# Optimization experiments

Measured on AMD Instinct MI355X. Metric: run time of the kernel, lower is better.

## Reference

```python
import jax, jax.numpy as jnp
import numpy as np

UNITS = 1024
N_CLASSES = 16
F_IN = 128
LN_EPS = 1e-3  # keras LayerNormalization default epsilon


def _lstm_cell(x, h, c, W, U, b):
    # keras LSTMCell gate order: i, f, g(candidate), o
    z = x @ W + h @ U + b  # [B, 4U]
    i, f, g, o = jnp.split(z, 4, axis=-1)
    i = jax.nn.sigmoid(i)
    f = jax.nn.sigmoid(f)
    g = jnp.tanh(g)
    o = jax.nn.sigmoid(o)
    c_new = f * c + i * g
    h_new = o * jnp.tanh(c_new)
    return h_new, c_new


def _layernorm(x, gamma, beta):
    mu = jnp.mean(x, axis=-1, keepdims=True)
    var = jnp.mean(jnp.square(x - mu), axis=-1, keepdims=True)
    return (x - mu) * jax.lax.rsqrt(var + LN_EPS) * gamma + beta


def setup_inputs() -> dict:
    key = jax.random.key(0)
    ks = jax.random.split(key, 8)
    s = 0.02
    inp = {
        "inputs": jax.random.normal(ks[0], (64, 512, F_IN), dtype=jnp.float32),
        "W0": jax.random.normal(ks[1], (F_IN, 4 * UNITS), dtype=jnp.float32) * s,
        "U0": jax.random.normal(ks[2], (UNITS, 4 * UNITS), dtype=jnp.float32) * s,
        "b0": jnp.zeros((4 * UNITS,), jnp.float32),
        "g0": jnp.ones((UNITS,), jnp.float32),
        "be0": jnp.zeros((UNITS,), jnp.float32),
        "W1": jax.random.normal(ks[3], (UNITS, 4 * UNITS), dtype=jnp.float32) * s,
        "U1": jax.random.normal(ks[4], (UNITS, 4 * UNITS), dtype=jnp.float32) * s,
        "b1": jnp.zeros((4 * UNITS,), jnp.float32),
        "g1": jnp.ones((UNITS,), jnp.float32),
        "be1": jnp.zeros((UNITS,), jnp.float32),
        "Wfc": jax.random.normal(ks[5], (UNITS, N_CLASSES), dtype=jnp.float32) * s,
        "bfc": jnp.zeros((N_CLASSES,), jnp.float32),
    }
    return inp


def reference(inputs, W0, U0, b0, g0, be0, W1, U1, b1, g1, be1, Wfc, bfc):
    B = inputs.shape[0]
    x_t = jnp.transpose(inputs, (1, 0, 2))  # [T, B, F]
    h0 = jnp.zeros((B, UNITS), jnp.float32)
    c0 = jnp.zeros((B, UNITS), jnp.float32)
    h1 = jnp.zeros((B, UNITS), jnp.float32)
    c1 = jnp.zeros((B, UNITS), jnp.float32)

    def step(carry, xt):
        h0, c0, h1, c1 = carry
        # layer 0: raw (h, c) carried across time; normalized output feeds layer 1
        h0n, c0n = _lstm_cell(xt, h0, c0, W0, U0, b0)
        o0 = _layernorm(h0n, g0, be0)
        h1n, c1n = _lstm_cell(o0, h1, c1, W1, U1, b1)
        o1 = _layernorm(h1n, g1, be1)
        # dropout is identity at inference (training=False)
        logits = jax.nn.softmax(o1 @ Wfc + bfc, axis=-1)
        return (h0n, c0n, h1n, c1n), logits

    _, out = jax.lax.scan(step, (h0, c0, h1, c1), x_t)  # [T, B, C]
    return jnp.transpose(out, (1, 0, 2))  # [B, T, C]
```

## Files before the change

### kernel.cpp

```cpp
#include <hip/hip_runtime.h>

typedef unsigned short u16;
typedef unsigned int u32;
typedef unsigned long long u64;
typedef __bf16 bf16x8 __attribute__((ext_vector_type(8)));
typedef float f32x4 __attribute__((ext_vector_type(4)));

#define T_LEN 512
#define BATCH 64
#define FIN 128
#define UNITS 1024

#define O_BAR   0
#define SZ_BAR  8192
#define O_XBF   SZ_BAR
#define SZ_XBF  (T_LEN*BATCH*FIN*2)
#define O_WP0   (O_XBF + SZ_XBF)
#define SZ_WP0  (1152*4096*2)
#define O_WP1   (O_WP0 + SZ_WP0)
#define SZ_WP1  (2048*4096*2)
#define O_WFC   (O_WP1 + SZ_WP1)
#define SZ_WFC  (16*1024*2)
#define O_H0    (O_WFC + SZ_WFC)
#define SZ_H    (BATCH*UNITS*2)
#define O_H1    (O_H0 + SZ_H)
#define WS_NEED (O_H1 + SZ_H)

__device__ __forceinline__ float bf2f(u16 s) {
  u32 u = ((u32)s) << 16;
  return __builtin_bit_cast(float, u);
}
__device__ __forceinline__ u16 f2bf(float f) {
  u32 u = __builtin_bit_cast(u32, f);
  u32 r = (u + 0x7FFFu + ((u >> 16) & 1u)) >> 16;
  return (u16)r;
}
__device__ __forceinline__ float sigm(float x) { return 1.0f / (1.0f + __expf(-x)); }
__device__ __forceinline__ float tanhft(float x) { return 1.0f - 2.0f / (__expf(2.0f * x) + 1.0f); }

__device__ __forceinline__ uint4 ldh16(const u16* q) {
  u64 a = __hip_atomic_load((const u64*)q,     __ATOMIC_RELAXED, __HIP_MEMORY_SCOPE_AGENT);
  u64 b = __hip_atomic_load((const u64*)q + 1, __ATOMIC_RELAXED, __HIP_MEMORY_SCOPE_AGENT);
  uint4 r; r.x = (u32)a; r.y = (u32)(a >> 32); r.z = (u32)b; r.w = (u32)(b >> 32);
  return r;
}
__device__ __forceinline__ void sth(u16* q, u16 v) {
  __hip_atomic_store(q, v, __ATOMIC_RELAXED, __HIP_MEMORY_SCOPE_AGENT);
}

__global__ void k_zero(u32* p, int n) {
  int i = blockIdx.x * 256 + threadIdx.x;
  if (i < n) p[i] = 0u;
}

__global__ void k_pack_x(const float* __restrict__ src, u16* __restrict__ dst) {
  int i = blockIdx.x * 256 + threadIdx.x;
  int f = i & 127, tb = i >> 7;
  int b = tb & 63, t = tb >> 6;
  dst[i] = f2bf(src[(b * T_LEN + t) * FIN + f]);
}

__global__ void k_pack_w0(const float* __restrict__ W0, const float* __restrict__ U0,
                          u16* __restrict__ dst) {
  int i = blockIdx.x * 256 + threadIdx.x;
  int j = i & 7, lane = (i >> 3) & 63, rest = i >> 9;
  int ktg = rest % 36, tmp = rest / 36;
  int nt = tmp & 3, ug = tmp >> 2;
  int k = ktg * 32 + ((lane >> 4) << 3) + j;
  int rr = nt * 16 + (lane & 15);
  int gate = rr & 3, ul = rr >> 2;
  int col = gate * 1024 + ug * 16 + ul;
  float v = (k < FIN) ? W0[k * 4096 + col] : U0[(k - FIN) * 4096 + col];
  dst[i] = f2bf(v);
}

__global__ void k_pack_w1(const float* __restrict__ W1, const float* __restrict__ U1,
                          u16* __restrict__ dst) {
  int i = blockIdx.x * 256 + threadIdx.x;
  int j = i & 7, lane = (i >> 3) & 63, rest = i >> 9;
  int ktg = rest & 63, tmp = rest >> 6;
  int nt = tmp & 3, ug = tmp >> 2;
  int k = ktg * 32 + ((lane >> 4) << 3) + j;
  int rr = nt * 16 + (lane & 15);
  int gate = rr & 3, ul = rr >> 2;
  int col = gate * 1024 + ug * 16 + ul;
  float v = (k < UNITS) ? W1[k * 4096 + col] : U1[(k - UNITS) * 4096 + col];
  dst[i] = f2bf(v);
}

__global__ void k_pack_wfc(const float* __restrict__ Wfc, u16* __restrict__ dst) {
  int i = blockIdx.x * 256 + threadIdx.x;
  int k = i & 1023, c = i >> 10;
  dst[c * 1024 + k] = f2bf(Wfc[k * 16 + c]);
}

struct KP {
  const u16* xbf; const u16* wp0; const u16* wp1; const u16* wfc;
  u16* h0; u16* h1; u32* bar;
  const float* b0; const float* g0; const float* be0;
  const float* b1; const float* g1; const float* be1;
  const float* bfc; float* out;
};

__device__ __forceinline__ void accst(uint4 v, float& s1, float& s2) {
  u32 a[4] = {v.x, v.y, v.z, v.w};
#pragma unroll
  for (int e = 0; e < 4; ++e) {
    float f0 = bf2f((u16)(a[e] & 0xffffu));
    float f1 = bf2f((u16)(a[e] >> 16));
    s1 += f0 + f1;
    s2 += f0 * f0 + f1 * f1;
  }
}

__device__ __forceinline__ uint4 normpack(uint4 v, float mu, float rs,
                                          const float* gg, const float* bb) {
  u32 a[4] = {v.x, v.y, v.z, v.w};
  u32 o[4];
#pragma unroll
  for (int e = 0; e < 4; ++e) {
    float f0 = (bf2f((u16)(a[e] & 0xffffu)) - mu) * rs * gg[2 * e] + bb[2 * e];
    float f1 = (bf2f((u16)(a[e] >> 16)) - mu) * rs * gg[2 * e + 1] + bb[2 * e + 1];
    o[e] = (u32)f2bf(f0) | ((u32)f2bf(f1) << 16);
  }
  uint4 r; r.x = o[0]; r.y = o[1]; r.z = o[2]; r.w = o[3];
  return r;
}

__device__ __forceinline__ void barrier_bg(u32* gen, u32* flags, int ug, int lane,
                                           int wv, u32 ep) {
  __syncthreads();
  if (wv == 0) {
    if (lane == 0)
      __hip_atomic_store(flags + ug * 4, ep, __ATOMIC_RELAXED, __HIP_MEMORY_SCOPE_AGENT);
    if (ug == 0) {
      for (;;) {
        u32 v = __hip_atomic_load(flags + lane * 4, __ATOMIC_RELAXED, __HIP_MEMORY_SCOPE_AGENT);
        if (__ballot(v >= ep) == ~0ull) break;
        __builtin_amdgcn_s_sleep(1);
      }
      if (lane == 0)
        __hip_atomic_store(gen, ep, __ATOMIC_RELAXED, __HIP_MEMORY_SCOPE_AGENT);
    } else if (lane == 0) {
      while (__hip_atomic_load(gen, __ATOMIC_RELAXED, __HIP_MEMORY_SCOPE_AGENT) < ep)
        __builtin_amdgcn_s_sleep(1);
    }
  }
  __syncthreads();
  asm volatile("" ::: "memory");
}

__global__ void __launch_bounds__(512, 2) k_persist(KP p) {
  const int tid = threadIdx.x;
  const int ug = blockIdx.x & 63, bg = blockIdx.x >> 6;
  const int lane = tid & 63, wv = tid >> 6;
  const int nt = wv & 3, kh = wv >> 2;

  __shared__ __align__(16) u16 bufA[16][1032];
  __shared__ __align__(16) u16 bufB[16][1032];
  __shared__ __align__(16) u16 buf0[16][1032];
  __shared__ float zb[2][16][68];
  __shared__ float g0s[1024], be0s[1024];
  __shared__ float b0s[64], b1s[64];
  __shared__ float mu_s[16], sg_s[16];
  __shared__ float lbuf[16];

  for (int i = tid; i < 1024; i += 512) { g0s[i] = p.g0[i]; be0s[i] = p.be0[i]; }
  if (tid < 64) {
    int gate = tid & 3, ul = tid >> 2;
    b0s[tid] = p.b0[gate * 1024 + ug * 16 + ul];
    b1s[tid] = p.b1[gate * 1024 + ug * 16 + ul];
  }
  {
    u32* za = (u32*)&bufA[0][0];
    u32* zc = (u32*)&bufB[0][0];
    for (int i = tid; i < 16 * 1032 / 2; i += 512) { za[i] = 0u; zc[i] = 0u; }
  }
  const float g1a = p.g1[tid * 2], g1b = p.g1[tid * 2 + 1];
  const float be1a = p.be1[tid * 2], be1b = p.be1[tid * 2 + 1];

  bf16x8 w0r[18], w1r[32];
  {
    const u16* q0 = p.wp0 + (size_t)(((ug * 4 + nt) * 36 + kh * 18) * 64 + lane) * 8;
#pragma unroll
    for (int s = 0; s < 18; ++s)
      w0r[s] = __builtin_bit_cast(bf16x8, *(const uint4*)(q0 + (size_t)s * 512));
    const u16* q1 = p.wp1 + (size_t)(((ug * 4 + nt) * 64 + kh * 32) * 64 + lane) * 8;
#pragma unroll
    for (int s = 0; s < 32; ++s)
      w1r[s] = __builtin_bit_cast(bf16x8, *(const uint4*)(q1 + (size_t)s * 512));
  }

  u32* gen   = p.bar + bg * 64;
  u32* flags = p.bar + 256 + bg * 256;

  float c0 = 0.f, c1 = 0.f;
  const int gr = tid >> 4, gu = tid & 15;
  const int srow = tid >> 5, ssub = tid & 31;
  const int am = lane & 15, aq = (lane >> 4) << 3;

  __syncthreads();

  for (int t = 0; t < T_LEN; ++t) {
    const u32 epA = 2 * t + 1, epB = 2 * t + 2;

    f32x4 acc0 = {0.f, 0.f, 0.f, 0.f};
    if (kh == 0) {
      const u16* xr = p.xbf + (size_t)(t * 64 + bg * 16 + am) * FIN + aq;
#pragma unroll
      for (int s = 0; s < 4; ++s) {
        bf16x8 a = __builtin_bit_cast(bf16x8, *(const uint4*)(xr + s * 32));
        acc0 = __builtin_amdgcn_mfma_f32_16x16x32_bf16(a, w0r[s], acc0, 0, 0, 0);
      }
#pragma unroll
      for (int s = 4; s < 18; ++s) {
        bf16x8 a = __builtin_bit_cast(bf16x8, *(const uint4*)&bufA[am][s * 32 + aq - 128]);
        acc0 = __builtin_amdgcn_mfma_f32_16x16x32_bf16(a, w0r[s], acc0, 0, 0, 0);
      }
    } else {
#pragma unroll
      for (int s = 0; s < 18; ++s) {
        bf16x8 a = __builtin_bit_cast(bf16x8, *(const uint4*)&bufA[am][448 + s * 32 + aq]);
        acc0 = __builtin_amdgcn_mfma_f32_16x16x32_bf16(a, w0r[s], acc0, 0, 0, 0);
      }
    }
#pragma unroll
    for (int i = 0; i < 4; ++i)
      zb[kh][(lane >> 4) * 4 + i][nt * 16 + (lane & 15)] = acc0[i];
    __syncthreads();

    if (tid < 256) {
      const float* zr0 = &zb[0][gr][gu * 4];
      const float* zr1 = &zb[1][gr][gu * 4];
      float zi = zr0[0] + zr1[0] + b0s[gu * 4 + 0];
      float zf = zr0[1] + zr1[1] + b0s[gu * 4 + 1];
      float zg = zr0[2] + zr1[2] + b0s[gu * 4 + 2];
      float zo = zr0[3] + zr1[3] + b0s[gu * 4 + 3];
      float gi = sigm(zi), gf = sigm(zf), gg = tanhft(zg), go = sigm(zo);
      c0 = gf * c0 + gi * gg;
      float h = go * tanhft(c0);
      sth(p.h0 + (size_t)(bg * 16 + gr) * UNITS + ug * 16 + gu, f2bf(h));
    }
    barrier_bg(gen, flags, ug, lane, wv, epA);

    {
      const u16* h0r = p.h0 + (size_t)(bg * 16 + srow) * UNITS + ssub * 8;
      uint4 a0 = ldh16(h0r);
      uint4 a1 = ldh16(h0r + 256);
      uint4 a2 = ldh16(h0r + 512);
      uint4 a3 = ldh16(h0r + 768);

      float s1 = 0.f, s2 = 0.f;
      accst(a0, s1, s2); accst(a1, s1, s2); accst(a2, s1, s2); accst(a3, s1, s2);
#pragma unroll
      for (int m = 1; m <= 16; m <<= 1) { s1 += __shfl_xor(s1, m); s2 += __shfl_xor(s2, m); }
      if (ssub == 0) {
        float mu = s1 * (1.0f / 1024.0f);
        float va = s2 * (1.0f / 1024.0f) - mu * mu;
        mu_s[srow] = mu;
        sg_s[srow] = rsqrtf(va + 1e-3f);
      }
      *(uint4*)&bufA[srow][ssub * 8]       = a0;
      *(uint4*)&bufA[srow][256 + ssub * 8] = a1;
      *(uint4*)&bufA[srow][512 + ssub * 8] = a2;
      *(uint4*)&bufA[srow][768 + ssub * 8] = a3;
      __syncthreads();
      float mu = mu_s[srow], rs = sg_s[srow];
      *(uint4*)&buf0[srow][ssub * 8]       = normpack(a0, mu, rs, &g0s[ssub * 8], &be0s[ssub * 8]);
      *(uint4*)&buf0[srow][256 + ssub * 8] = normpack(a1, mu, rs, &g0s[256 + ssub * 8], &be0s[256 + ssub * 8]);
      *(uint4*)&buf0[srow][512 + ssub * 8] = normpack(a2, mu, rs, &g0s[512 + ssub * 8], &be0s[512 + ssub * 8]);
      *(uint4*)&buf0[srow][768 + ssub * 8] = normpack(a3, mu, rs, &g0s[768 + ssub * 8], &be0s[768 + ssub * 8]);
    }
    __syncthreads();

    f32x4 acc1 = {0.f, 0.f, 0.f, 0.f};
    if (kh == 0) {
#pragma unroll
      for (int s = 0; s < 32; ++s) {
        bf16x8 a = __builtin_bit_cast(bf16x8, *(const uint4*)&buf0[am][s * 32 + aq]);
        acc1 = __builtin_amdgcn_mfma_f32_16x16x32_bf16(a, w1r[s], acc1, 0, 0, 0);
      }
    } else {
#pragma unroll
      for (int s = 0; s < 32; ++s) {
        bf16x8 a = __builtin_bit_cast(bf16x8, *(const uint4*)&bufB[am][s * 32 + aq]);
        acc1 = __builtin_amdgcn_mfma_f32_16x16x32_bf16(a, w1r[s], acc1, 0, 0, 0);
      }
    }
#pragma unroll
    for (int i = 0; i < 4; ++i)
      zb[kh][(lane >> 4) * 4 + i][nt * 16 + (lane & 15)] = acc1[i];
    __syncthreads();

    if (tid < 256) {
      const float* zr0 = &zb[0][gr][gu * 4];
      const float* zr1 = &zb[1][gr][gu * 4];
      float zi = zr0[0] + zr1[0] + b1s[gu * 4 + 0];
      float zf = zr0[1] + zr1[1] + b1s[gu * 4 + 1];
      float zg = zr0[2] + zr1[2] + b1s[gu * 4 + 2];
      float zo = zr0[3] + zr1[3] + b1s[gu * 4 + 3];
      float gi = sigm(zi), gf = sigm(zf), gg = tanhft(zg), go = sigm(zo);
      c1 = gf * c1 + gi * gg;
      float h = go * tanhft(c1);
      sth(p.h1 + (size_t)(bg * 16 + gr) * UNITS + ug * 16 + gu, f2bf(h));
    }
    barrier_bg(gen, flags, ug, lane, wv, epB);

    {
      const u16* h1r = p.h1 + (size_t)(bg * 16 + srow) * UNITS + ssub * 8;
      uint4 a0 = ldh16(h1r);
      uint4 a1 = ldh16(h1r + 256);
      uint4 a2 = ldh16(h1r + 512);
      uint4 a3 = ldh16(h1r + 768);
      float s1 = 0.f, s2 = 0.f;
      accst(a0, s1, s2); accst(a1, s1, s2); accst(a2, s1, s2); accst(a3, s1, s2);
#pragma unroll
      for (int m = 1; m <= 16; m <<= 1) { s1 += __shfl_xor(s1, m); s2 += __shfl_xor(s2, m); }
      if (ssub == 0) {
        float mu = s1 * (1.0f / 1024.0f);
        float va = s2 * (1.0f / 1024.0f) - mu * mu;
        mu_s[srow] = mu;
        sg_s[srow] = rsqrtf(va + 1e-3f);
      }
      *(uint4*)&bufB[srow][ssub * 8]       = a0;
      *(uint4*)&bufB[srow][256 + ssub * 8] = a1;
      *(uint4*)&bufB[srow][512 + ssub * 8] = a2;
      *(uint4*)&bufB[srow][768 + ssub * 8] = a3;
    }
    __syncthreads();

    if (ug < 16) {
      const int row = bg * 16 + ug;
      u32 hv = *(const u32*)&bufB[ug][tid * 2];
      float f0 = bf2f((u16)(hv & 0xffffu)), f1 = bf2f((u16)(hv >> 16));
      {
        float mu = mu_s[ug], rs = sg_s[ug];
        float* o1f = (float*)&buf0[0][0];
        o1f[tid * 2]     = (f0 - mu) * rs * g1a + be1a;
        o1f[tid * 2 + 1] = (f1 - mu) * rs * g1b + be1b;
      }
      __syncthreads();
      if (tid < 256) {
        const int cls = tid & 15, ks = tid >> 4;
        const float* o1f = (const float*)&buf0[0][0];
        const u16* wrow = p.wfc + cls * 1024 + ks * 64;
        float pa = 0.f;
#pragma unroll
        for (int q8 = 0; q8 < 8; ++q8) {
          uint4 wv4 = *(const uint4*)(wrow + q8 * 8);
          u32 aa[4] = {wv4.x, wv4.y, wv4.z, wv4.w};
#pragma unroll
          for (int e = 0; e < 4; ++e) {
            int k = ks * 64 + q8 * 8 + e * 2;
            pa += o1f[k]     * bf2f((u16)(aa[e] & 0xffffu));
            pa += o1f[k + 1] * bf2f((u16)(aa[e] >> 16));
          }
        }
        zb[0][ks][cls] = pa;
      }
      __syncthreads();
      if (tid < 16) {
        float lg = p.bfc[tid];
#pragma unroll
        for (int ks = 0; ks < 16; ++ks) lg += zb[0][ks][tid];
        lbuf[tid] = lg;
      }
      __syncthreads();
      if (tid < 16) {
        float mx = lbuf[0];
#pragma unroll
        for (int j2 = 1; j2 < 16; ++j2) mx = fmaxf(mx, lbuf[j2]);
        float ssum = 0.f;
#pragma unroll
        for (int j2 = 0; j2 < 16; ++j2) ssum += __expf(lbuf[j2] - mx);
        p.out[((size_t)row * T_LEN + t) * 16 + tid] = __expf(lbuf[tid] - mx) / ssum;
      }
      __syncthreads();
    }
  }
}

extern "C" void kernel_launch(void* const* d_in, const int* in_sizes, int n_in,
                              void* d_out, int out_size, void* d_ws, size_t ws_size,
                              hipStream_t stream) {
  (void)in_sizes; (void)n_in; (void)out_size;
  if (ws_size < (size_t)WS_NEED) return;

  const float* inp = (const float*)d_in[0];
  const float* W0  = (const float*)d_in[1];
  const float* U0  = (const float*)d_in[2];
  const float* b0  = (const float*)d_in[3];
  const float* g0  = (const float*)d_in[4];
  const float* be0 = (const float*)d_in[5];
  const float* W1  = (const float*)d_in[6];
  const float* U1  = (const float*)d_in[7];
  const float* b1  = (const float*)d_in[8];
  const float* g1  = (const float*)d_in[9];
  const float* be1 = (const float*)d_in[10];
  const float* Wfc = (const float*)d_in[11];
  const float* bfc = (const float*)d_in[12];

  char* ws = (char*)d_ws;
  u32* bar  = (u32*)(ws + O_BAR);
  u16* xbf  = (u16*)(ws + O_XBF);
  u16* wp0  = (u16*)(ws + O_WP0);
  u16* wp1  = (u16*)(ws + O_WP1);
  u16* wfcT = (u16*)(ws + O_WFC);
  u16* h0   = (u16*)(ws + O_H0);
  u16* h1   = (u16*)(ws + O_H1);

  k_zero<<<8, 256, 0, stream>>>(bar, 2048);
  k_pack_x<<<16384, 256, 0, stream>>>(inp, xbf);
  k_pack_w0<<<18432, 256, 0, stream>>>(W0, U0, wp0);
  k_pack_w1<<<32768, 256, 0, stream>>>(W1, U1, wp1);
  k_pack_wfc<<<64, 256, 0, stream>>>(Wfc, wfcT);

  KP p;
  p.xbf = xbf; p.wp0 = wp0; p.wp1 = wp1; p.wfc = wfcT;
  p.h0 = h0; p.h1 = h1; p.bar = bar;
  p.b0 = b0; p.g0 = g0; p.be0 = be0;
  p.b1 = b1; p.g1 = g1; p.be1 = be1;
  p.bfc = bfc; p.out = (float*)d_out;

  void* args[] = { &p };
  hipLaunchCooperativeKernel((const void*)k_persist, dim3(256), dim3(512), args, 0, stream);
}
```

Measured before the change: 7.683 ms.

## Merge per-step grid barriers via double-buffered hidden states and decentralized barrier

Double-buffers the h0/h1 global hidden-state buffers by timestep parity, so the layer-1 state from the previous step can be read after the same barrier that publishes the current layer-0 state. This halves the group-wide barriers per timestep from two to one. The barrier also becomes decentralized: every block polls all flags itself instead of waiting for a leader block to set a generation word. The FC/softmax output is deferred one step, with an epilogue barrier for the last step. The cost is extra polling traffic on the flags from every block and a more subtle ordering argument for buffer reuse across steps.

```diff
diff --git a/kernel.cpp b/kernel.cpp
--- a/kernel.cpp
+++ b/kernel.cpp
@@ -10,6 +10,7 @@
 #define BATCH 64
 #define FIN 128
 #define UNITS 1024
+#define H_STRIDE 65536
 
 #define O_BAR   0
 #define SZ_BAR  8192
@@ -22,7 +23,7 @@
 #define O_WFC   (O_WP1 + SZ_WP1)
 #define SZ_WFC  (16*1024*2)
 #define O_H0    (O_WFC + SZ_WFC)
-#define SZ_H    (BATCH*UNITS*2)
+#define SZ_H    (2*H_STRIDE*2)
 #define O_H1    (O_H0 + SZ_H)
 #define WS_NEED (O_H1 + SZ_H)
 
@@ -127,27 +128,73 @@
   return r;
 }
 
-__device__ __forceinline__ void barrier_bg(u32* gen, u32* flags, int ug, int lane,
-                                           int wv, u32 ep) {
+__device__ __forceinline__ void barrier_bg(u32* flags, int ug, int lane, int wv, u32 ep) {
   __syncthreads();
   if (wv == 0) {
     if (lane == 0)
       __hip_atomic_store(flags + ug * 4, ep, __ATOMIC_RELAXED, __HIP_MEMORY_SCOPE_AGENT);
-    if (ug == 0) {
-      for (;;) {
-        u32 v = __hip_atomic_load(flags + lane * 4, __ATOMIC_RELAXED, __HIP_MEMORY_SCOPE_AGENT);
-        if (__ballot(v >= ep) == ~0ull) break;
-        __builtin_amdgcn_s_sleep(1);
-      }
-      if (lane == 0)
-        __hip_atomic_store(gen, ep, __ATOMIC_RELAXED, __HIP_MEMORY_SCOPE_AGENT);
-    } else if (lane == 0) {
-      while (__hip_atomic_load(gen, __ATOMIC_RELAXED, __HIP_MEMORY_SCOPE_AGENT) < ep)
-        __builtin_amdgcn_s_sleep(1);
+    for (;;) {
+      u32 v = __hip_atomic_load(flags + lane * 4, __ATOMIC_RELAXED, __HIP_MEMORY_SCOPE_AGENT);
+      if (__ballot(v >= ep) == ~0ull) break;
+      __builtin_amdgcn_s_sleep(1);
     }
   }
   __syncthreads();
   asm volatile("" ::: "memory");
+}
+
+__device__ __forceinline__ void fc_out(int tid, int ug, int bg, int t,
+    u16 (*bufB)[1032], u16 (*buf0)[1032], float (*zb0)[68],
+    const float* mu_s, const float* sg_s, float* lbuf,
+    float g1a, float g1b, float be1a, float be1b,
+    const u16* __restrict__ wfc, const float* __restrict__ bfc,
+    float* __restrict__ out) {
+  const int row = bg * 16 + ug;
+  u32 hv = *(const u32*)&bufB[ug][tid * 2];
+  float f0 = bf2f((u16)(hv & 0xffffu)), f1 = bf2f((u16)(hv >> 16));
+  {
+    float mu = mu_s[ug], rs = sg_s[ug];
+    float* o1f = (float*)&buf0[0][0];
+    o1f[tid * 2]     = (f0 - mu) * rs * g1a + be1a;
+    o1f[tid * 2 + 1] = (f1 - mu) * rs * g1b + be1b;
+  }
+  __syncthreads();
+  if (tid < 256) {
+    const int cls = tid & 15, ks = tid >> 4;
+    const float* o1f = (const float*)&buf0[0][0];
+    const u16* wrow = wfc + cls * 1024 + ks * 64;
+    float pa = 0.f;
+#pragma unroll
+    for (int q8 = 0; q8 < 8; ++q8) {
+      uint4 wv4 = *(const uint4*)(wrow + q8 * 8);
+      u32 aa[4] = {wv4.x, wv4.y, wv4.z, wv4.w};
+#pragma unroll
+      for (int e = 0; e < 4; ++e) {
+        int k = ks * 64 + q8 * 8 + e * 2;
+        pa += o1f[k]     * bf2f((u16)(aa[e] & 0xffffu));
+        pa += o1f[k + 1] * bf2f((u16)(aa[e] >> 16));
+      }
+    }
+    zb0[ks][cls] = pa;
+  }
+  __syncthreads();
+  if (tid < 16) {
+    float lg = bfc[tid];
+#pragma unroll
+    for (int ks = 0; ks < 16; ++ks) lg += zb0[ks][tid];
+    lbuf[tid] = lg;
+  }
+  __syncthreads();
+  if (tid < 16) {
+    float mx = lbuf[0];
+#pragma unroll
+    for (int j2 = 1; j2 < 16; ++j2) mx = fmaxf(mx, lbuf[j2]);
+    float ssum = 0.f;
+#pragma unroll
+    for (int j2 = 0; j2 < 16; ++j2) ssum += __expf(lbuf[j2] - mx);
+    out[((size_t)row * T_LEN + t) * 16 + tid] = __expf(lbuf[tid] - mx) / ssum;
+  }
+  __syncthreads();
 }
 
 __global__ void __launch_bounds__(512, 2) k_persist(KP p) {
@@ -173,8 +220,7 @@
   }
   {
     u32* za = (u32*)&bufA[0][0];
-    u32* zc = (u32*)&bufB[0][0];
-    for (int i = tid; i < 16 * 1032 / 2; i += 512) { za[i] = 0u; zc[i] = 0u; }
+    for (int i = tid; i < 16 * 1032 / 2; i += 512) za[i] = 0u;
   }
   const float g1a = p.g1[tid * 2], g1b = p.g1[tid * 2 + 1];
   const float be1a = p.be1[tid * 2], be1b = p.be1[tid * 2 + 1];
@@ -191,8 +237,7 @@
       w1r[s] = __builtin_bit_cast(bf16x8, *(const uint4*)(q1 + (size_t)s * 512));
   }
 
-  u32* gen   = p.bar + bg * 64;
-  u32* flags = p.bar + 256 + bg * 256;
+  u32* flags = p.bar + bg * 256;
 
   float c0 = 0.f, c1 = 0.f;
   const int gr = tid >> 4, gu = tid & 15;
@@ -202,7 +247,7 @@
   __syncthreads();
 
   for (int t = 0; t < T_LEN; ++t) {
-    const u32 epA = 2 * t + 1, epB = 2 * t + 2;
+    const int cur = t & 1, rd = cur ^ 1;
 
     f32x4 acc0 = {0.f, 0.f, 0.f, 0.f};
     if (kh == 0) {
@@ -239,37 +284,53 @@
       float gi = sigm(zi), gf = sigm(zf), gg = tanhft(zg), go = sigm(zo);
       c0 = gf * c0 + gi * gg;
       float h = go * tanhft(c0);
-      sth(p.h0 + (size_t)(bg * 16 + gr) * UNITS + ug * 16 + gu, f2bf(h));
-    }
-    barrier_bg(gen, flags, ug, lane, wv, epA);
+      sth(p.h0 + (size_t)cur * H_STRIDE + (size_t)(bg * 16 + gr) * UNITS + ug * 16 + gu,
+          f2bf(h));
+    }
+    barrier_bg(flags, ug, lane, wv, (u32)(t + 1));
 
     {
-      const u16* h0r = p.h0 + (size_t)(bg * 16 + srow) * UNITS + ssub * 8;
+      const u16* h0r = p.h0 + (size_t)cur * H_STRIDE + (size_t)(bg * 16 + srow) * UNITS + ssub * 8;
+      const u16* h1r = p.h1 + (size_t)rd  * H_STRIDE + (size_t)(bg * 16 + srow) * UNITS + ssub * 8;
       uint4 a0 = ldh16(h0r);
       uint4 a1 = ldh16(h0r + 256);
       uint4 a2 = ldh16(h0r + 512);
       uint4 a3 = ldh16(h0r + 768);
+      uint4 b0 = ldh16(h1r);
+      uint4 b1 = ldh16(h1r + 256);
+      uint4 b2 = ldh16(h1r + 512);
+      uint4 b3 = ldh16(h1r + 768);
 
       float s1 = 0.f, s2 = 0.f;
       accst(a0, s1, s2); accst(a1, s1, s2); accst(a2, s1, s2); accst(a3, s1, s2);
 #pragma unroll
       for (int m = 1; m <= 16; m <<= 1) { s1 += __shfl_xor(s1, m); s2 += __shfl_xor(s2, m); }
-      if (ssub == 0) {
-        float mu = s1 * (1.0f / 1024.0f);
-        float va = s2 * (1.0f / 1024.0f) - mu * mu;
-        mu_s[srow] = mu;
-        sg_s[srow] = rsqrtf(va + 1e-3f);
-      }
+      float mu0 = s1 * (1.0f / 1024.0f);
+      float rs0 = rsqrtf(s2 * (1.0f / 1024.0f) - mu0 * mu0 + 1e-3f);
+
       *(uint4*)&bufA[srow][ssub * 8]       = a0;
       *(uint4*)&bufA[srow][256 + ssub * 8] = a1;
       *(uint4*)&bufA[srow][512 + ssub * 8] = a2;
       *(uint4*)&bufA[srow][768 + ssub * 8] = a3;
-      __syncthreads();
-      float mu = mu_s[srow], rs = sg_s[srow];
-      *(uint4*)&buf0[srow][ssub * 8]       = normpack(a0, mu, rs, &g0s[ssub * 8], &be0s[ssub * 8]);
-      *(uint4*)&buf0[srow][256 + ssub * 8] = normpack(a1, mu, rs, &g0s[256 + ssub * 8], &be0s[256 + ssub * 8]);
-      *(uint4*)&buf0[srow][512 + ssub * 8] = normpack(a2, mu, rs, &g0s[512 + ssub * 8], &be0s[512 + ssub * 8]);
-      *(uint4*)&buf0[srow][768 + ssub * 8] = normpack(a3, mu, rs, &g0s[768 + ssub * 8], &be0s[768 + ssub * 8]);
+
+      float u1 = 0.f, u2 = 0.f;
+      accst(b0, u1, u2); accst(b1, u1, u2); accst(b2, u1, u2); accst(b3, u1, u2);
+#pragma unroll
+      for (int m = 1; m <= 16; m <<= 1) { u1 += __shfl_xor(u1, m); u2 += __shfl_xor(u2, m); }
+      if (ssub == 0) {
+        float mu = u1 * (1.0f / 1024.0f);
+        mu_s[srow] = mu;
+        sg_s[srow] = rsqrtf(u2 * (1.0f / 1024.0f) - mu * mu + 1e-3f);
+      }
+      *(uint4*)&bufB[srow][ssub * 8]       = b0;
+      *(uint4*)&bufB[srow][256 + ssub * 8] = b1;
+      *(uint4*)&bufB[srow][512 + ssub * 8] = b2;
+      *(uint4*)&bufB[srow][768 + ssub * 8] = b3;
+
+      *(uint4*)&buf0[srow][ssub * 8]       = normpack(a0, mu0, rs0, &g0s[ssub * 8], &be0s[ssub * 8]);
+      *(uint4*)&buf0[srow][256 + ssub * 8] = normpack(a1, mu0, rs0, &g0s[256 + ssub * 8], &be0s[256 + ssub * 8]);
+      *(uint4*)&buf0[srow][512 + ssub * 8] = normpack(a2, mu0, rs0, &g0s[512 + ssub * 8], &be0s[512 + ssub * 8]);
+      *(uint4*)&buf0[srow][768 + ssub * 8] = normpack(a3, mu0, rs0, &g0s[768 + ssub * 8], &be0s[768 + ssub * 8]);
     }
     __syncthreads();
 
@@ -302,82 +363,41 @@
       float gi = sigm(zi), gf = sigm(zf), gg = tanhft(zg), go = sigm(zo);
       c1 = gf * c1 + gi * gg;
       float h = go * tanhft(c1);
-      sth(p.h1 + (size_t)(bg * 16 + gr) * UNITS + ug * 16 + gu, f2bf(h));
-    }
-    barrier_bg(gen, flags, ug, lane, wv, epB);
-
-    {
-      const u16* h1r = p.h1 + (size_t)(bg * 16 + srow) * UNITS + ssub * 8;
-      uint4 a0 = ldh16(h1r);
-      uint4 a1 = ldh16(h1r + 256);
-      uint4 a2 = ldh16(h1r + 512);
-      uint4 a3 = ldh16(h1r + 768);
-      float s1 = 0.f, s2 = 0.f;
-      accst(a0, s1, s2); accst(a1, s1, s2); accst(a2, s1, s2); accst(a3, s1, s2);
-#pragma unroll
-      for (int m = 1; m <= 16; m <<= 1) { s1 += __shfl_xor(s1, m); s2 += __shfl_xor(s2, m); }
-      if (ssub == 0) {
-        float mu = s1 * (1.0f / 1024.0f);
-        float va = s2 * (1.0f / 1024.0f) - mu * mu;
-        mu_s[srow] = mu;
-        sg_s[srow] = rsqrtf(va + 1e-3f);
-      }
-      *(uint4*)&bufB[srow][ssub * 8]       = a0;
-      *(uint4*)&bufB[srow][256 + ssub * 8] = a1;
-      *(uint4*)&bufB[srow][512 + ssub * 8] = a2;
-      *(uint4*)&bufB[srow][768 + ssub * 8] = a3;
-    }
-    __syncthreads();
-
-    if (ug < 16) {
-      const int row = bg * 16 + ug;
-      u32 hv = *(const u32*)&bufB[ug][tid * 2];
-      float f0 = bf2f((u16)(hv & 0xffffu)), f1 = bf2f((u16)(hv >> 16));
-      {
-        float mu = mu_s[ug], rs = sg_s[ug];
-        float* o1f = (float*)&buf0[0][0];
-        o1f[tid * 2]     = (f0 - mu) * rs * g1a + be1a;
-        o1f[tid * 2 + 1] = (f1 - mu) * rs * g1b + be1b;
-      }
-      __syncthreads();
-      if (tid < 256) {
-        const int cls = tid & 15, ks = tid >> 4;
-        const float* o1f = (const float*)&buf0[0][0];
-        const u16* wrow = p.wfc + cls * 1024 + ks * 64;
-        float pa = 0.f;
-#pragma unroll
-        for (int q8 = 0; q8 < 8; ++q8) {
-          uint4 wv4 = *(const uint4*)(wrow + q8 * 8);
-          u32 aa[4] = {wv4.x, wv4.y, wv4.z, wv4.w};
-#pragma unroll
-          for (int e = 0; e < 4; ++e) {
-            int k = ks * 64 + q8 * 8 + e * 2;
-            pa += o1f[k]     * bf2f((u16)(aa[e] & 0xffffu));
-            pa += o1f[k + 1] * bf2f((u16)(aa[e] >> 16));
-          }
-        }
-        zb[0][ks][cls] = pa;
-      }
-      __syncthreads();
-      if (tid < 16) {
-        float lg = p.bfc[tid];
-#pragma unroll
-        for (int ks = 0; ks < 16; ++ks) lg += zb[0][ks][tid];
-        lbuf[tid] = lg;
-      }
-      __syncthreads();
-      if (tid < 16) {
-        float mx = lbuf[0];
-#pragma unroll
-        for (int j2 = 1; j2 < 16; ++j2) mx = fmaxf(mx, lbuf[j2]);
-        float ssum = 0.f;
-#pragma unroll
-        for (int j2 = 0; j2 < 16; ++j2) ssum += __expf(lbuf[j2] - mx);
-        p.out[((size_t)row * T_LEN + t) * 16 + tid] = __expf(lbuf[tid] - mx) / ssum;
-      }
-      __syncthreads();
-    }
-  }
+      sth(p.h1 + (size_t)cur * H_STRIDE + (size_t)(bg * 16 + gr) * UNITS + ug * 16 + gu,
+          f2bf(h));
+    }
+
+    if (ug < 16 && t > 0)
+      fc_out(tid, ug, bg, t - 1, bufB, buf0, zb[0], mu_s, sg_s, lbuf,
+             g1a, g1b, be1a, be1b, p.wfc, p.bfc, p.out);
+  }
+
+  barrier_bg(flags, ug, lane, wv, (u32)(T_LEN + 1));
+  {
+    const u16* h1r = p.h1 + (size_t)((T_LEN - 1) & 1) * H_STRIDE
+                   + (size_t)(bg * 16 + srow) * UNITS + ssub * 8;
+    uint4 b0 = ldh16(h1r);
+    uint4 b1 = ldh16(h1r + 256);
+    uint4 b2 = ldh16(h1r + 512);
+    uint4 b3 = ldh16(h1r + 768);
+    float u1 = 0.f, u2 = 0.f;
+    accst(b0, u1, u2); accst(b1, u1, u2); accst(b2, u1, u2); accst(b3, u1, u2);
+#pragma unroll
+    for (int m = 1; m <= 16; m <<= 1) { u1 += __shfl_xor(u1, m); u2 += __shfl_xor(u2, m); }
+    if (ssub == 0) {
+      float mu = u1 * (1.0f / 1024.0f);
+      mu_s[srow] = mu;
+      sg_s[srow] = rsqrtf(u2 * (1.0f / 1024.0f) - mu * mu + 1e-3f);
+    }
+    *(uint4*)&bufB[srow][ssub * 8]       = b0;
+    *(uint4*)&bufB[srow][256 + ssub * 8] = b1;
+    *(uint4*)&bufB[srow][512 + ssub * 8] = b2;
+    *(uint4*)&bufB[srow][768 + ssub * 8] = b3;
+  }
+  __syncthreads();
+  if (ug < 16)
+    fc_out(tid, ug, bg, T_LEN - 1, bufB, buf0, zb[0], mu_s, sg_s, lbuf,
+           g1a, g1b, be1a, be1b, p.wfc, p.bfc, p.out);
 }
 
 extern "C" void kernel_launch(void* const* d_in, const int* in_sizes, int n_in,
@@ -410,6 +430,7 @@
   u16* h1   = (u16*)(ws + O_H1);
 
   k_zero<<<8, 256, 0, stream>>>(bar, 2048);
+  k_zero<<<512, 256, 0, stream>>>((u32*)(ws + O_H0), (SZ_H + SZ_H) / 4);
   k_pack_x<<<16384, 256, 0, stream>>>(inp, xbf);
   k_pack_w0<<<18432, 256, 0, stream>>>(W0, U0, wp0);
   k_pack_w1<<<32768, 256, 0, stream>>>(W1, U1, wp1);
```

New measurement: 9.390 ms. +22.2%, slower.
